# Kernel optimization log

Hardware: AMD Instinct MI355X
Metric: run time of the kernel (lower is better)

Reference implementation:

```python
import jax, jax.numpy as jnp
import numpy as np

B, T, E, H, L, V, CTX = 16, 1024, 512, 8, 6, 32, 1024
HD = E // H


def setup_inputs() -> dict:
    key = jax.random.key(0)
    ks = jax.random.split(key, 20)
    s = 0.02
    inp = {
        "tokens": jax.random.randint(ks[0], (B, T), 0, V),
        "emb": jax.random.normal(ks[1], (V, E), jnp.float32) * s,
        "pos_emb": jax.random.normal(ks[2], (CTX, E), jnp.float32) * s,
        "Wq": jax.random.normal(ks[3], (L, H, E, HD), jnp.float32) * s,
        "Wk": jax.random.normal(ks[4], (L, H, E, HD), jnp.float32) * s,
        "Wv": jax.random.normal(ks[5], (L, H, E, HD), jnp.float32) * s,
        "Wo": jax.random.normal(ks[6], (L, E, E), jnp.float32) * s,
        "bo": jnp.zeros((L, E), jnp.float32),
        "ln1_g": jnp.ones((L, E), jnp.float32),
        "ln1_b": jnp.zeros((L, E), jnp.float32),
        "ln2_g": jnp.ones((L, E), jnp.float32),
        "ln2_b": jnp.zeros((L, E), jnp.float32),
        "W1": jax.random.normal(ks[7], (L, E, E), jnp.float32) * s,
        "b1": jnp.zeros((L, E), jnp.float32),
        "W2": jax.random.normal(ks[8], (L, E, E), jnp.float32) * s,
        "b2": jnp.zeros((L, E), jnp.float32),
        "lnf_g": jnp.ones((E,), jnp.float32),
        "lnf_b": jnp.zeros((E,), jnp.float32),
        "Wf": jax.random.normal(ks[9], (E, V), jnp.float32) * s,
        "bf": jnp.zeros((V,), jnp.float32),
    }
    return inp


def _layernorm(x, g, b, eps=1e-5):
    mu = x.mean(-1, keepdims=True)
    var = ((x - mu) ** 2).mean(-1, keepdims=True)
    return (x - mu) * jax.lax.rsqrt(var + eps) * g + b


def reference(tokens, emb, pos_emb, Wq, Wk, Wv, Wo, bo, ln1_g, ln1_b,
              ln2_g, ln2_b, W1, b1, W2, b2, lnf_g, lnf_b, Wf, bf):
    Bt, Tt = tokens.shape
    x = emb[tokens] + pos_emb[:Tt]  # [B,T,E]
    causal = jnp.tril(jnp.ones((Tt, Tt), bool))

    def block(x, p):
        wq, wk, wv, wo, bo_, g1, b1_, g2, b2_, w1, bb1, w2, bb2 = p
        h = _layernorm(x, g1, b1_)
        q = jnp.einsum('bte,hed->bhtd', h, wq)
        k = jnp.einsum('bte,hed->bhtd', h, wk)
        v = jnp.einsum('bte,hed->bhtd', h, wv)
        # NOTE: source applies NO 1/sqrt(d) scaling
        s = jnp.einsum('bhtd,bhsd->bhts', q, k)
        s = jnp.where(causal, s, -jnp.inf)
        a = jax.nn.softmax(s, axis=-1)
        o = jnp.einsum('bhts,bhsd->bhtd', a, v)
        o = o.transpose(0, 2, 1, 3).reshape(Bt, Tt, E)  # concat heads
        x = x + jnp.einsum('bte,ef->btf', o, wo) + bo_
        h2 = _layernorm(x, g2, b2_)
        f = jax.nn.relu(jnp.einsum('bte,ef->btf', h2, w1) + bb1)
        f = jnp.einsum('bte,ef->btf', f, w2) + bb2
        return x + f, None

    x, _ = jax.lax.scan(block, x, (Wq, Wk, Wv, Wo, bo, ln1_g, ln1_b,
                                   ln2_g, ln2_b, W1, b1, W2, b2))
    x = _layernorm(x, lnf_g, lnf_b)
    logits = jnp.einsum('bte,ev->btv', x, Wf) + bf
    return logits
```

## Files before the change

### kernel.cpp

```cpp
#include <hip/hip_runtime.h>
#include <hip/hip_bf16.h>

namespace {

constexpr int B = 16, T = 1024, E = 512, H = 8, L = 6, V = 32, HD = 64;
constexpr int BT = B * T;
constexpr long S = (long)BT * E;

typedef __attribute__((ext_vector_type(8))) short bf16x8;
typedef __attribute__((ext_vector_type(4))) float f32x4;

__device__ inline float b2f(ushort u) {
  union { unsigned u; float f; } v; v.u = (unsigned)u << 16; return v.f;
}
__device__ inline ushort f2b(float f) {
  union { float f; unsigned u; } v; v.f = f;
  unsigned r = v.u + 0x7FFFu + ((v.u >> 16) & 1u);
  return (ushort)(r >> 16);
}
__device__ inline void gl_lds16(const ushort* g, ushort* lds) {
  __builtin_amdgcn_global_load_lds(
      (const __attribute__((address_space(1))) void*)g,
      (__attribute__((address_space(3))) void*)lds, 16, 0, 0);
}

__global__ void embed_kernel(const int* __restrict__ tokens,
                             const float* __restrict__ emb,
                             const float* __restrict__ pos,
                             float* __restrict__ x) {
  int idx = blockIdx.x * blockDim.x + threadIdx.x;
  constexpr int TOT = BT * (E / 4);
  if (idx >= TOT) return;
  int row = idx >> 7, c4 = idx & 127;
  int t = row & (T - 1);
  int tok = tokens[row];
  float4 a = reinterpret_cast<const float4*>(emb + (long)tok * E)[c4];
  float4 p = reinterpret_cast<const float4*>(pos + (long)t * E)[c4];
  float4 r;
  r.x = a.x + p.x; r.y = a.y + p.y; r.z = a.z + p.z; r.w = a.w + p.w;
  reinterpret_cast<float4*>(x + (long)row * E)[c4] = r;
}

__global__ __launch_bounds__(256)
void wconv_kernel(const float* __restrict__ in, ushort* __restrict__ out,
                  int K, int Nn) {
  const long pbase = (long)blockIdx.z * K * Nn;
  __shared__ float t[32][33];
  const int k0 = blockIdx.x * 32, n0 = blockIdx.y * 32;
  const int tid = threadIdx.x, r = tid >> 5, c = tid & 31;
  #pragma unroll
  for (int i = 0; i < 4; i++)
    t[r + i * 8][c] = in[pbase + (long)(k0 + r + i * 8) * Nn + n0 + c];
  __syncthreads();
  #pragma unroll
  for (int i = 0; i < 4; i++)
    out[pbase + (long)(n0 + r + i * 8) * K + k0 + c] = f2b(t[c][r + i * 8]);
}

__global__ __launch_bounds__(128)
void ln_kernel(const float* __restrict__ x, const float* __restrict__ g,
               const float* __restrict__ b, ushort* __restrict__ out) {
  int row = blockIdx.x, tid = threadIdx.x;
  float4 v = reinterpret_cast<const float4*>(x + (long)row * E)[tid];
  float s = v.x + v.y + v.z + v.w;
  #pragma unroll
  for (int off = 32; off > 0; off >>= 1) s += __shfl_down(s, off, 64);
  __shared__ float r1[2], r2[2];
  int lane = tid & 63, wid = tid >> 6;
  if (lane == 0) r1[wid] = s;
  __syncthreads();
  float mean = (r1[0] + r1[1]) * (1.0f / E);
  float4 d;
  d.x = v.x - mean; d.y = v.y - mean; d.z = v.z - mean; d.w = v.w - mean;
  float s2 = d.x * d.x + d.y * d.y + d.z * d.z + d.w * d.w;
  #pragma unroll
  for (int off = 32; off > 0; off >>= 1) s2 += __shfl_down(s2, off, 64);
  if (lane == 0) r2[wid] = s2;
  __syncthreads();
  float rstd = rsqrtf((r2[0] + r2[1]) * (1.0f / E) + 1e-5f);
  float4 gg = reinterpret_cast<const float4*>(g)[tid];
  float4 bb = reinterpret_cast<const float4*>(b)[tid];
  ushort4 o;
  o.x = f2b(d.x * rstd * gg.x + bb.x);
  o.y = f2b(d.y * rstd * gg.y + bb.y);
  o.z = f2b(d.z * rstd * gg.z + bb.z);
  o.w = f2b(d.w * rstd * gg.w + bb.w);
  reinterpret_cast<ushort4*>(out + (long)row * E)[tid] = o;
}

template <int MODE>
__global__ __launch_bounds__(256, 2)
void bgemm_kernel(const ushort* __restrict__ A, const ushort* __restrict__ Bt,
                  const float* __restrict__ bias, const float* __restrict__ res,
                  void* __restrict__ Cout) {
  constexpr int K = 512, N = 512;
  __shared__ ushort As[128][32];
  __shared__ ushort Bs[128][32];
  const int tid = threadIdx.x, lane = tid & 63, wid = tid >> 6;
  const int bm = blockIdx.x * 128, bn = blockIdx.y * 128;
  const int wm = (wid >> 1) * 64, wn = (wid & 1) * 64;
  const int lo = lane & 15, hi = lane >> 4;
  const int arow = lane >> 2, acol = (lane & 3) * 8;
  f32x4 acc[4][4] = {};
  for (int k0 = 0; k0 < K; k0 += 32) {
    #pragma unroll
    for (int i = 0; i < 2; i++) {
      int seg = wid * 2 + i;
      gl_lds16(A + (long)(bm + seg * 16 + arow) * K + k0 + acol,
               &As[seg * 16][0]);
      gl_lds16(Bt + (long)(bn + seg * 16 + arow) * K + k0 + acol,
               &Bs[seg * 16][0]);
    }
    __syncthreads();
    bf16x8 af[4], bfr[4];
    #pragma unroll
    for (int mi = 0; mi < 4; mi++)
      af[mi] = *(const bf16x8*)&As[wm + mi * 16 + lo][hi * 8];
    #pragma unroll
    for (int ni = 0; ni < 4; ni++)
      bfr[ni] = *(const bf16x8*)&Bs[wn + ni * 16 + lo][hi * 8];
    #pragma unroll
    for (int mi = 0; mi < 4; mi++)
      #pragma unroll
      for (int ni = 0; ni < 4; ni++)
        acc[mi][ni] = __builtin_amdgcn_mfma_f32_16x16x32_bf16(
            af[mi], bfr[ni], acc[mi][ni], 0, 0, 0);
    __syncthreads();
  }
  #pragma unroll
  for (int mi = 0; mi < 4; mi++) {
    #pragma unroll
    for (int ni = 0; ni < 4; ni++) {
      const int gn = bn + wn + ni * 16 + lo;
      const float bv = (MODE >= 1) ? bias[gn] : 0.f;
      #pragma unroll
      for (int r = 0; r < 4; r++) {
        const long gm = bm + wm + mi * 16 + hi * 4 + r;
        float vv = acc[mi][ni][r];
        if (MODE == 0) {
          ((ushort*)Cout)[gm * N + gn] = f2b(vv);
        } else if (MODE == 1) {
          ((float*)Cout)[gm * N + gn] = vv + bv + res[gm * N + gn];
        } else {
          ((ushort*)Cout)[gm * N + gn] = f2b(fmaxf(vv + bv, 0.f));
        }
      }
    }
  }
}

__global__ __launch_bounds__(256, 2)
void attn_kernel(const ushort* __restrict__ q, const ushort* __restrict__ k,
                 const ushort* __restrict__ v, ushort* __restrict__ o) {
  const int b = blockIdx.z, h = blockIdx.y;
  const int qt = (gridDim.x - 1) - blockIdx.x;
  const int tid = threadIdx.x, wid = tid >> 6, lane = tid & 63;
  const int lo = lane & 15, hi = lane >> 4;
  const long bh = (long)b * T;
  const int qbase = qt * 128 + wid * 32;
  const int dch = qt * 2 + (wid >> 1);
  const int roff = 32 * (wid & 1);
  __shared__ ushort Ks[64 * 64];
  __shared__ ushort Vs[64 * 64];
  __shared__ ushort Ps[4][32 * 64];
  char* KsB = (char*)Ks;
  char* VsB = (char*)Vs;
  char* PsB = (char*)Ps[wid];

  bf16x8 qf[2][2];
  #pragma unroll
  for (int mf = 0; mf < 2; mf++)
    #pragma unroll
    for (int kh = 0; kh < 2; kh++)
      qf[mf][kh] = *(const bf16x8*)(q + (bh + qbase + mf * 16 + lo) * E +
                                    h * 64 + kh * 32 + hi * 8);
  f32x4 accO[2][4] = {};
  float m[2][4], lsum[2][4];
  #pragma unroll
  for (int a = 0; a < 2; a++)
    #pragma unroll
    for (int r = 0; r < 4; r++) { m[a][r] = -1e30f; lsum[a][r] = 0.f; }

  const ushort* kb = k + bh * E + h * 64;
  const ushort* vb = v + bh * E + h * 64;
  const int nch = qt * 2 + 2;

  for (int c = 0; c < nch; c++) {
    const long s0 = (long)c * 64;
    #pragma unroll
    for (int it = 0; it < 2; it++) {
      int idx = it * 256 + tid;
      int key = idx >> 3, c8 = idx & 7;
      uint4 kv = *(const uint4*)(kb + (s0 + key) * E + c8 * 8);
      *(uint4*)(KsB + ((key * 128 + c8 * 16) ^ ((key & 7) << 4))) = kv;
    }
    {
      const int key0 = (tid & 31) * 2, dim0 = (tid >> 5) * 8;
      uint4 v0 = *(const uint4*)(vb + (s0 + key0) * E + dim0);
      uint4 v1 = *(const uint4*)(vb + (s0 + key0 + 1) * E + dim0);
      const ushort* p0 = (const ushort*)&v0;
      const ushort* p1 = (const ushort*)&v1;
      #pragma unroll
      for (int j = 0; j < 8; j++) {
        const int dim = dim0 + j;
        ushort2 w;
        w.x = p0[j]; w.y = p1[j];
        *(ushort2*)(VsB + ((dim * 128 + key0 * 2) ^ ((dim & 7) << 4))) = w;
      }
    }
    __syncthreads();
    if (c <= dch) {
      const bool diag = (c == dch);
      bf16x8 kf[4][2];
      #pragma unroll
      for (int nf = 0; nf < 4; nf++)
        #pragma unroll
        for (int kh = 0; kh < 2; kh++) {
          const int key = nf * 16 + lo;
          kf[nf][kh] = *(const bf16x8*)(
              KsB + ((key * 128 + kh * 64 + hi * 16) ^ ((key & 7) << 4)));
        }
      #pragma unroll
      for (int mf = 0; mf < 2; mf++) {
        f32x4 s[4];
        #pragma unroll
        for (int nf = 0; nf < 4; nf++) {
          f32x4 z = {0.f, 0.f, 0.f, 0.f};
          z = __builtin_amdgcn_mfma_f32_16x16x32_bf16(qf[mf][0], kf[nf][0],
                                                      z, 0, 0, 0);
          z = __builtin_amdgcn_mfma_f32_16x16x32_bf16(qf[mf][1], kf[nf][1],
                                                      z, 0, 0, 0);
          s[nf] = z;
        }
        if (diag) {
          #pragma unroll
          for (int nf = 0; nf < 4; nf++)
            #pragma unroll
            for (int r = 0; r < 4; r++)
              if (nf * 16 + lo > roff + mf * 16 + hi * 4 + r)
                s[nf][r] = -1e30f;
        }
        #pragma unroll
        for (int r = 0; r < 4; r++) {
          float pm = fmaxf(fmaxf(s[0][r], s[1][r]), fmaxf(s[2][r], s[3][r]));
          #pragma unroll
          for (int msk = 1; msk < 16; msk <<= 1)
            pm = fmaxf(pm, __shfl_xor(pm, msk, 64));
          const float mn = fmaxf(m[mf][r], pm);
          const float sc = __expf(m[mf][r] - mn);
          m[mf][r] = mn;
          float p0 = __expf(s[0][r] - mn), p1 = __expf(s[1][r] - mn);
          float p2 = __expf(s[2][r] - mn), p3 = __expf(s[3][r] - mn);
          lsum[mf][r] = lsum[mf][r] * sc + (p0 + p1 + p2 + p3);
          #pragma unroll
          for (int nd = 0; nd < 4; nd++) accO[mf][nd][r] *= sc;
          const int ql = mf * 16 + hi * 4 + r;
          const int swz = (ql & 7) << 4;
          *(ushort*)(PsB + ((ql * 128 + (lo) * 2) ^ swz))      = f2b(p0);
          *(ushort*)(PsB + ((ql * 128 + (16 + lo) * 2) ^ swz)) = f2b(p1);
          *(ushort*)(PsB + ((ql * 128 + (32 + lo) * 2) ^ swz)) = f2b(p2);
          *(ushort*)(PsB + ((ql * 128 + (48 + lo) * 2) ^ swz)) = f2b(p3);
        }
      }
      asm volatile("s_waitcnt lgkmcnt(0)" ::: "memory");
      #pragma unroll
      for (int ks = 0; ks < 2; ks++) {
        bf16x8 pa[2];
        #pragma unroll
        for (int mf = 0; mf < 2; mf++) {
          const int ql = mf * 16 + lo;
          pa[mf] = *(const bf16x8*)(
              PsB + ((ql * 128 + ks * 64 + hi * 16) ^ ((ql & 7) << 4)));
        }
        #pragma unroll
        for (int nd = 0; nd < 4; nd++) {
          const int dim = nd * 16 + lo;
          bf16x8 vf = *(const bf16x8*)(
              VsB + ((dim * 128 + ks * 64 + hi * 16) ^ ((dim & 7) << 4)));
          #pragma unroll
          for (int mf = 0; mf < 2; mf++)
            accO[mf][nd] = __builtin_amdgcn_mfma_f32_16x16x32_bf16(
                pa[mf], vf, accO[mf][nd], 0, 0, 0);
        }
      }
    }
    __syncthreads();
  }
  #pragma unroll
  for (int mf = 0; mf < 2; mf++)
    #pragma unroll
    for (int r = 0; r < 4; r++) {
      float l = lsum[mf][r];
      #pragma unroll
      for (int msk = 1; msk < 16; msk <<= 1) l += __shfl_xor(l, msk, 64);
      lsum[mf][r] = 1.0f / l;
    }
  #pragma unroll
  for (int mf = 0; mf < 2; mf++)
    #pragma unroll
    for (int nd = 0; nd < 4; nd++)
      #pragma unroll
      for (int r = 0; r < 4; r++) {
        const int ql = mf * 16 + hi * 4 + r, dim = nd * 16 + lo;
        *(ushort*)(PsB + ql * 128 + dim * 2) =
            f2b(accO[mf][nd][r] * lsum[mf][r]);
      }
  asm volatile("s_waitcnt lgkmcnt(0)" ::: "memory");
  #pragma unroll
  for (int it = 0; it < 4; it++) {
    const int idx = it * 64 + lane;
    const int row = idx >> 3, c8 = idx & 7;
    uint4 val = *(const uint4*)(PsB + row * 128 + c8 * 16);
    *(uint4*)(o + (bh + qbase + row) * E + h * 64 + c8 * 8) = val;
  }
}

__global__ __launch_bounds__(256)
void logits_kernel(const ushort* __restrict__ xf, const ushort* __restrict__ WfT,
                   const float* __restrict__ bf, float* __restrict__ out) {
  __shared__ float xs[8][E];
  const int row0 = blockIdx.x * 8, tid = threadIdx.x;
  #pragma unroll
  for (int i = 0; i < 4; i++) {
    int idx = i * 256 + tid;
    int r = idx >> 7, c4 = idx & 127;
    ushort4 u = ((const ushort4*)(xf + (long)(row0 + r) * E))[c4];
    float4 f;
    f.x = b2f(u.x); f.y = b2f(u.y); f.z = b2f(u.z); f.w = b2f(u.w);
    *(float4*)&xs[r][c4 * 4] = f;
  }
  __syncthreads();
  const int r = tid >> 5, c = tid & 31;
  float acc = 0.f;
  for (int e8 = 0; e8 < 64; e8++) {
    uint4 w = *(const uint4*)(WfT + (long)c * E + e8 * 8);
    const ushort* ws = (const ushort*)&w;
    #pragma unroll
    for (int j = 0; j < 8; j++) acc += xs[r][e8 * 8 + j] * b2f(ws[j]);
  }
  out[(long)(row0 + r) * V + c] = acc + bf[c];
}

}

extern "C" void kernel_launch(void* const* d_in, const int* in_sizes, int n_in,
                              void* d_out, int out_size, void* d_ws,
                              size_t ws_size, hipStream_t stream) {
  const int*   tokens = (const int*)d_in[0];
  const float* emb    = (const float*)d_in[1];
  const float* pos    = (const float*)d_in[2];
  const float* Wq     = (const float*)d_in[3];
  const float* Wk     = (const float*)d_in[4];
  const float* Wv     = (const float*)d_in[5];
  const float* Wo     = (const float*)d_in[6];
  const float* bo     = (const float*)d_in[7];
  const float* ln1g   = (const float*)d_in[8];
  const float* ln1b   = (const float*)d_in[9];
  const float* ln2g   = (const float*)d_in[10];
  const float* ln2b   = (const float*)d_in[11];
  const float* W1     = (const float*)d_in[12];
  const float* b1     = (const float*)d_in[13];
  const float* W2     = (const float*)d_in[14];
  const float* b2     = (const float*)d_in[15];
  const float* lnfg   = (const float*)d_in[16];
  const float* lnfb   = (const float*)d_in[17];
  const float* Wf     = (const float*)d_in[18];
  const float* bf     = (const float*)d_in[19];
  float* out = (float*)d_out;

  char* p = (char*)d_ws;
  float*  x   = (float*)p;           p += S * 4;
  ushort* hb  = (ushort*)p;          p += S * 2;
  ushort* qbb = (ushort*)p;          p += S * 2;
  ushort* kbb = (ushort*)p;          p += S * 2;
  ushort* vbb = (ushort*)p;          p += S * 2;
  const long WSZ = (long)L * E * E;
  ushort* wqT = (ushort*)p;          p += WSZ * 2;
  ushort* wkT = (ushort*)p;          p += WSZ * 2;
  ushort* wvT = (ushort*)p;          p += WSZ * 2;
  ushort* woT = (ushort*)p;          p += WSZ * 2;
  ushort* w1T = (ushort*)p;          p += WSZ * 2;
  ushort* w2T = (ushort*)p;          p += WSZ * 2;
  ushort* wfT = (ushort*)p;          p += (long)E * V * 2;

  wconv_kernel<<<dim3(16, 2, L * H), 256, 0, stream>>>(Wq, wqT, E, HD);
  wconv_kernel<<<dim3(16, 2, L * H), 256, 0, stream>>>(Wk, wkT, E, HD);
  wconv_kernel<<<dim3(16, 2, L * H), 256, 0, stream>>>(Wv, wvT, E, HD);
  wconv_kernel<<<dim3(16, 16, L), 256, 0, stream>>>(Wo, woT, E, E);
  wconv_kernel<<<dim3(16, 16, L), 256, 0, stream>>>(W1, w1T, E, E);
  wconv_kernel<<<dim3(16, 16, L), 256, 0, stream>>>(W2, w2T, E, E);
  wconv_kernel<<<dim3(16, 1, 1), 256, 0, stream>>>(Wf, wfT, E, V);

  embed_kernel<<<(BT * (E / 4) + 255) / 256, 256, 0, stream>>>(tokens, emb,
                                                               pos, x);

  const dim3 gg(BT / 128, E / 128);
  const dim3 ga(T / 128, H, B);

  for (int l = 0; l < L; l++) {
    const long wo = (long)l * E * E;
    ln_kernel<<<BT, 128, 0, stream>>>(x, ln1g + l * E, ln1b + l * E, hb);
    bgemm_kernel<0><<<gg, 256, 0, stream>>>(hb, wqT + wo, nullptr, nullptr,
                                            qbb);
    bgemm_kernel<0><<<gg, 256, 0, stream>>>(hb, wkT + wo, nullptr, nullptr,
                                            kbb);
    bgemm_kernel<0><<<gg, 256, 0, stream>>>(hb, wvT + wo, nullptr, nullptr,
                                            vbb);
    attn_kernel<<<ga, 256, 0, stream>>>(qbb, kbb, vbb, hb);
    bgemm_kernel<1><<<gg, 256, 0, stream>>>(hb, woT + wo, bo + l * E, x, x);
    ln_kernel<<<BT, 128, 0, stream>>>(x, ln2g + l * E, ln2b + l * E, hb);
    bgemm_kernel<2><<<gg, 256, 0, stream>>>(hb, w1T + wo, b1 + l * E, nullptr,
                                            qbb);
    bgemm_kernel<1><<<gg, 256, 0, stream>>>(qbb, w2T + wo, b2 + l * E, x, x);
  }

  ln_kernel<<<BT, 128, 0, stream>>>(x, lnfg, lnfb, hb);
  logits_kernel<<<BT / 8, 256, 0, stream>>>(hb, wfT, bf, out);
}
```

Measured before the change: 1.578 ms.

## Fuse QKV projections into one GEMM and double-buffer attention K/V tiles

The three Q/K/V weight matrices are packed into a single transposed [1536x512] weight per layer, so one GEMM launch writes an interleaved QKV buffer. The attention kernel now reads from that strided buffer and double-buffers its K/V shared-memory tiles, prefetching the next chunk into registers while computing the current one. It also raises wave priority around MFMA bursts. This removes two GEMM launches per layer and hides global-load latency in attention, at the cost of more LDS and registers per block, which may lower occupancy.

```diff
diff --git a/kernel.cpp b/kernel.cpp
--- a/kernel.cpp
+++ b/kernel.cpp
@@ -6,6 +6,7 @@
 constexpr int B = 16, T = 1024, E = 512, H = 8, L = 6, V = 32, HD = 64;
 constexpr int BT = B * T;
 constexpr long S = (long)BT * E;
+constexpr int QS = 1536;
 
 typedef __attribute__((ext_vector_type(8))) short bf16x8;
 typedef __attribute__((ext_vector_type(4))) float f32x4;
@@ -43,18 +44,21 @@
 
 __global__ __launch_bounds__(256)
 void wconv_kernel(const float* __restrict__ in, ushort* __restrict__ out,
-                  int K, int Nn) {
-  const long pbase = (long)blockIdx.z * K * Nn;
+                  int K, int Nn, int ppl, long layer_stride, long off) {
+  const int z = blockIdx.z;
+  const long pin = (long)z * K * Nn;
+  const long pout = (long)(z / ppl) * layer_stride + off +
+                    (long)(z % ppl) * Nn * K;
   __shared__ float t[32][33];
   const int k0 = blockIdx.x * 32, n0 = blockIdx.y * 32;
   const int tid = threadIdx.x, r = tid >> 5, c = tid & 31;
   #pragma unroll
   for (int i = 0; i < 4; i++)
-    t[r + i * 8][c] = in[pbase + (long)(k0 + r + i * 8) * Nn + n0 + c];
+    t[r + i * 8][c] = in[pin + (long)(k0 + r + i * 8) * Nn + n0 + c];
   __syncthreads();
   #pragma unroll
   for (int i = 0; i < 4; i++)
-    out[pbase + (long)(n0 + r + i * 8) * K + k0 + c] = f2b(t[c][r + i * 8]);
+    out[pout + (long)(n0 + r + i * 8) * K + k0 + c] = f2b(t[c][r + i * 8]);
 }
 
 __global__ __launch_bounds__(128)
@@ -92,8 +96,8 @@
 __global__ __launch_bounds__(256, 2)
 void bgemm_kernel(const ushort* __restrict__ A, const ushort* __restrict__ Bt,
                   const float* __restrict__ bias, const float* __restrict__ res,
-                  void* __restrict__ Cout) {
-  constexpr int K = 512, N = 512;
+                  void* __restrict__ Cout, int Nl) {
+  constexpr int K = 512;
   __shared__ ushort As[128][32];
   __shared__ ushort Bs[128][32];
   const int tid = threadIdx.x, lane = tid & 63, wid = tid >> 6;
@@ -138,11 +142,11 @@
         const long gm = bm + wm + mi * 16 + hi * 4 + r;
         float vv = acc[mi][ni][r];
         if (MODE == 0) {
-          ((ushort*)Cout)[gm * N + gn] = f2b(vv);
+          ((ushort*)Cout)[gm * Nl + gn] = f2b(vv);
         } else if (MODE == 1) {
-          ((float*)Cout)[gm * N + gn] = vv + bv + res[gm * N + gn];
+          ((float*)Cout)[gm * Nl + gn] = vv + bv + res[gm * Nl + gn];
         } else {
-          ((ushort*)Cout)[gm * N + gn] = f2b(fmaxf(vv + bv, 0.f));
+          ((ushort*)Cout)[gm * Nl + gn] = f2b(fmaxf(vv + bv, 0.f));
         }
       }
     }
@@ -150,8 +154,7 @@
 }
 
 __global__ __launch_bounds__(256, 2)
-void attn_kernel(const ushort* __restrict__ q, const ushort* __restrict__ k,
-                 const ushort* __restrict__ v, ushort* __restrict__ o) {
+void attn_kernel(const ushort* __restrict__ qkv, ushort* __restrict__ o) {
   const int b = blockIdx.z, h = blockIdx.y;
   const int qt = (gridDim.x - 1) - blockIdx.x;
   const int tid = threadIdx.x, wid = tid >> 6, lane = tid & 63;
@@ -160,11 +163,9 @@
   const int qbase = qt * 128 + wid * 32;
   const int dch = qt * 2 + (wid >> 1);
   const int roff = 32 * (wid & 1);
-  __shared__ ushort Ks[64 * 64];
-  __shared__ ushort Vs[64 * 64];
+  __shared__ ushort Ks[2][64 * 64];
+  __shared__ ushort Vs[2][64 * 64];
   __shared__ ushort Ps[4][32 * 64];
-  char* KsB = (char*)Ks;
-  char* VsB = (char*)Vs;
   char* PsB = (char*)Ps[wid];
 
   bf16x8 qf[2][2];
@@ -172,7 +173,7 @@
   for (int mf = 0; mf < 2; mf++)
     #pragma unroll
     for (int kh = 0; kh < 2; kh++)
-      qf[mf][kh] = *(const bf16x8*)(q + (bh + qbase + mf * 16 + lo) * E +
+      qf[mf][kh] = *(const bf16x8*)(qkv + (bh + qbase + mf * 16 + lo) * QS +
                                     h * 64 + kh * 32 + hi * 8);
   f32x4 accO[2][4] = {};
   float m[2][4], lsum[2][4];
@@ -181,35 +182,48 @@
     #pragma unroll
     for (int r = 0; r < 4; r++) { m[a][r] = -1e30f; lsum[a][r] = 0.f; }
 
-  const ushort* kb = k + bh * E + h * 64;
-  const ushort* vb = v + bh * E + h * 64;
+  const ushort* kb = qkv + bh * QS + 512 + h * 64;
+  const ushort* vb = qkv + bh * QS + 1024 + h * 64;
   const int nch = qt * 2 + 2;
 
+  uint4 kpre[2], vpre[2];
+  const int kkey0 = tid >> 3, kc8 = tid & 7;
+  const int vkey0 = (tid & 31) * 2, vdim0 = (tid >> 5) * 8;
+  auto LOADC = [&](int cc) {
+    const long s0 = (long)cc * 64;
+    kpre[0] = *(const uint4*)(kb + (s0 + kkey0) * QS + kc8 * 8);
+    kpre[1] = *(const uint4*)(kb + (s0 + kkey0 + 32) * QS + kc8 * 8);
+    vpre[0] = *(const uint4*)(vb + (s0 + vkey0) * QS + vdim0);
+    vpre[1] = *(const uint4*)(vb + (s0 + vkey0 + 1) * QS + vdim0);
+  };
+  auto WRITEC = [&](int buf) {
+    char* KsB = (char*)Ks[buf];
+    char* VsB = (char*)Vs[buf];
+    #pragma unroll
+    for (int it = 0; it < 2; it++) {
+      const int key = kkey0 + it * 32;
+      *(uint4*)(KsB + ((key * 128 + kc8 * 16) ^ ((key & 7) << 4))) = kpre[it];
+    }
+    const ushort* p0 = (const ushort*)&vpre[0];
+    const ushort* p1 = (const ushort*)&vpre[1];
+    #pragma unroll
+    for (int j = 0; j < 8; j++) {
+      const int dim = vdim0 + j;
+      ushort2 w; w.x = p0[j]; w.y = p1[j];
+      *(ushort2*)(VsB + ((dim * 128 + vkey0 * 2) ^ ((dim & 7) << 4))) = w;
+    }
+  };
+
+  LOADC(0);
+  WRITEC(0);
+  __syncthreads();
+
   for (int c = 0; c < nch; c++) {
-    const long s0 = (long)c * 64;
-    #pragma unroll
-    for (int it = 0; it < 2; it++) {
-      int idx = it * 256 + tid;
-      int key = idx >> 3, c8 = idx & 7;
-      uint4 kv = *(const uint4*)(kb + (s0 + key) * E + c8 * 8);
-      *(uint4*)(KsB + ((key * 128 + c8 * 16) ^ ((key & 7) << 4))) = kv;
-    }
-    {
-      const int key0 = (tid & 31) * 2, dim0 = (tid >> 5) * 8;
-      uint4 v0 = *(const uint4*)(vb + (s0 + key0) * E + dim0);
-      uint4 v1 = *(const uint4*)(vb + (s0 + key0 + 1) * E + dim0);
-      const ushort* p0 = (const ushort*)&v0;
-      const ushort* p1 = (const ushort*)&v1;
-      #pragma unroll
-      for (int j = 0; j < 8; j++) {
-        const int dim = dim0 + j;
-        ushort2 w;
-        w.x = p0[j]; w.y = p1[j];
-        *(ushort2*)(VsB + ((dim * 128 + key0 * 2) ^ ((dim & 7) << 4))) = w;
-      }
-    }
-    __syncthreads();
+    const int cur = c & 1;
+    if (c + 1 < nch) LOADC(c + 1);
     if (c <= dch) {
+      char* KsB = (char*)Ks[cur];
+      char* VsB = (char*)Vs[cur];
       const bool diag = (c == dch);
       bf16x8 kf[4][2];
       #pragma unroll
@@ -223,6 +237,7 @@
       #pragma unroll
       for (int mf = 0; mf < 2; mf++) {
         f32x4 s[4];
+        __builtin_amdgcn_s_setprio(1);
         #pragma unroll
         for (int nf = 0; nf < 4; nf++) {
           f32x4 z = {0.f, 0.f, 0.f, 0.f};
@@ -232,6 +247,7 @@
                                                       z, 0, 0, 0);
           s[nf] = z;
         }
+        __builtin_amdgcn_s_setprio(0);
         if (diag) {
           #pragma unroll
           for (int nf = 0; nf < 4; nf++)
@@ -272,6 +288,7 @@
           pa[mf] = *(const bf16x8*)(
               PsB + ((ql * 128 + ks * 64 + hi * 16) ^ ((ql & 7) << 4)));
         }
+        __builtin_amdgcn_s_setprio(1);
         #pragma unroll
         for (int nd = 0; nd < 4; nd++) {
           const int dim = nd * 16 + lo;
@@ -282,8 +299,10 @@
             accO[mf][nd] = __builtin_amdgcn_mfma_f32_16x16x32_bf16(
                 pa[mf], vf, accO[mf][nd], 0, 0, 0);
         }
+        __builtin_amdgcn_s_setprio(0);
       }
     }
+    if (c + 1 < nch) WRITEC(cur ^ 1);
     __syncthreads();
   }
   #pragma unroll
@@ -369,49 +388,53 @@
   float* out = (float*)d_out;
 
   char* p = (char*)d_ws;
-  float*  x   = (float*)p;           p += S * 4;
-  ushort* hb  = (ushort*)p;          p += S * 2;
-  ushort* qbb = (ushort*)p;          p += S * 2;
-  ushort* kbb = (ushort*)p;          p += S * 2;
-  ushort* vbb = (ushort*)p;          p += S * 2;
+  float*  x    = (float*)p;          p += S * 4;
+  ushort* hb   = (ushort*)p;         p += S * 2;
+  ushort* qkvb = (ushort*)p;         p += (long)BT * QS * 2;
   const long WSZ = (long)L * E * E;
-  ushort* wqT = (ushort*)p;          p += WSZ * 2;
-  ushort* wkT = (ushort*)p;          p += WSZ * 2;
-  ushort* wvT = (ushort*)p;          p += WSZ * 2;
-  ushort* woT = (ushort*)p;          p += WSZ * 2;
-  ushort* w1T = (ushort*)p;          p += WSZ * 2;
-  ushort* w2T = (ushort*)p;          p += WSZ * 2;
-  ushort* wfT = (ushort*)p;          p += (long)E * V * 2;
-
-  wconv_kernel<<<dim3(16, 2, L * H), 256, 0, stream>>>(Wq, wqT, E, HD);
-  wconv_kernel<<<dim3(16, 2, L * H), 256, 0, stream>>>(Wk, wkT, E, HD);
-  wconv_kernel<<<dim3(16, 2, L * H), 256, 0, stream>>>(Wv, wvT, E, HD);
-  wconv_kernel<<<dim3(16, 16, L), 256, 0, stream>>>(Wo, woT, E, E);
-  wconv_kernel<<<dim3(16, 16, L), 256, 0, stream>>>(W1, w1T, E, E);
-  wconv_kernel<<<dim3(16, 16, L), 256, 0, stream>>>(W2, w2T, E, E);
-  wconv_kernel<<<dim3(16, 1, 1), 256, 0, stream>>>(Wf, wfT, E, V);
+  ushort* wqkvT = (ushort*)p;        p += (long)L * QS * E * 2;
+  ushort* woT  = (ushort*)p;         p += WSZ * 2;
+  ushort* w1T  = (ushort*)p;         p += WSZ * 2;
+  ushort* w2T  = (ushort*)p;         p += WSZ * 2;
+  ushort* wfT  = (ushort*)p;         p += (long)E * V * 2;
+
+  const long QLS = (long)QS * E;
+
+  wconv_kernel<<<dim3(16, 2, L * H), 256, 0, stream>>>(Wq, wqkvT, E, HD, H,
+                                                       QLS, 0);
+  wconv_kernel<<<dim3(16, 2, L * H), 256, 0, stream>>>(Wk, wqkvT, E, HD, H,
+                                                       QLS, (long)512 * E);
+  wconv_kernel<<<dim3(16, 2, L * H), 256, 0, stream>>>(Wv, wqkvT, E, HD, H,
+                                                       QLS, (long)1024 * E);
+  wconv_kernel<<<dim3(16, 16, L), 256, 0, stream>>>(Wo, woT, E, E, 1,
+                                                    (long)E * E, 0);
+  wconv_kernel<<<dim3(16, 16, L), 256, 0, stream>>>(W1, w1T, E, E, 1,
+                                                    (long)E * E, 0);
+  wconv_kernel<<<dim3(16, 16, L), 256, 0, stream>>>(W2, w2T, E, E, 1,
+                                                    (long)E * E, 0);
+  wconv_kernel<<<dim3(16, 1, 1), 256, 0, stream>>>(Wf, wfT, E, V, 1,
+                                                   (long)E * V, 0);
 
   embed_kernel<<<(BT * (E / 4) + 255) / 256, 256, 0, stream>>>(tokens, emb,
                                                                pos, x);
 
+  const dim3 gq(BT / 128, QS / 128);
   const dim3 gg(BT / 128, E / 128);
   const dim3 ga(T / 128, H, B);
 
   for (int l = 0; l < L; l++) {
     const long wo = (long)l * E * E;
     ln_kernel<<<BT, 128, 0, stream>>>(x, ln1g + l * E, ln1b + l * E, hb);
-    bgemm_kernel<0><<<gg, 256, 0, stream>>>(hb, wqT + wo, nullptr, nullptr,
-                                            qbb);
-    bgemm_kernel<0><<<gg, 256, 0, stream>>>(hb, wkT + wo, nullptr, nullptr,
-                                            kbb);
-    bgemm_kernel<0><<<gg, 256, 0, stream>>>(hb, wvT + wo, nullptr, nullptr,
-                                            vbb);
-    attn_kernel<<<ga, 256, 0, stream>>>(qbb, kbb, vbb, hb);
-    bgemm_kernel<1><<<gg, 256, 0, stream>>>(hb, woT + wo, bo + l * E, x, x);
+    bgemm_kernel<0><<<gq, 256, 0, stream>>>(hb, wqkvT + l * QLS, nullptr,
+                                            nullptr, qkvb, QS);
+    attn_kernel<<<ga, 256, 0, stream>>>(qkvb, hb);
+    bgemm_kernel<1><<<gg, 256, 0, stream>>>(hb, woT + wo, bo + l * E, x, x,
+                                            E);
     ln_kernel<<<BT, 128, 0, stream>>>(x, ln2g + l * E, ln2b + l * E, hb);
     bgemm_kernel<2><<<gg, 256, 0, stream>>>(hb, w1T + wo, b1 + l * E, nullptr,
-                                            qbb);
-    bgemm_kernel<1><<<gg, 256, 0, stream>>>(qbb, w2T + wo, b2 + l * E, x, x);
+                                            qkvb, E);
+    bgemm_kernel<1><<<gg, 256, 0, stream>>>((ushort*)qkvb, w2T + wo,
+                                            b2 + l * E, x, x, E);
   }
 
   ln_kernel<<<BT, 128, 0, stream>>>(x, lnfg, lnfb, hb);
```

Result: no change. 1.557 ms (-1.3%).
